# Kernel tuning notes

Measured on AMD Instinct MI355X. Metric: run time of the kernel, lower is better.

Reference implementation:

```python
import jax, jax.numpy as jnp
import numpy as np

B, T, ENC, DEC, OUT = 4096, 128, 128, 128, 1


def setup_inputs() -> dict:
    key = jax.random.key(0)
    ks = jax.random.split(key, 10)
    def s(k, shape, scale):
        return jax.random.normal(k, shape, jnp.float32) * scale
    return {
        "input_encoded": jax.random.normal(ks[0], (B, T, ENC), jnp.float32),
        "y_history": jax.random.normal(ks[1], (B, T - 1, OUT), jnp.float32),
        # attn_layer: Linear(2*DEC+ENC -> ENC), Tanh, Linear(ENC -> 1)
        "attn_W1": s(ks[2], (ENC, 2 * DEC + ENC), 0.05),
        "attn_b1": jnp.zeros((ENC,), jnp.float32),
        "attn_W2": s(ks[3], (1, ENC), 0.05),
        "attn_b2": jnp.zeros((1,), jnp.float32),
        # LSTM(input_size=OUT, hidden_size=DEC), gate order i,f,g,o
        "W_ih": s(ks[4], (4 * DEC, OUT), 0.08),
        "W_hh": s(ks[5], (4 * DEC, DEC), 0.08),
        "b_ih": jnp.zeros((4 * DEC,), jnp.float32),
        "b_hh": jnp.zeros((4 * DEC,), jnp.float32),
        # fc: Linear(ENC+OUT -> OUT), weight initialized with normal_() (std 1)
        "fc_W": s(ks[6], (OUT, ENC + OUT), 1.0),
        "fc_b": jnp.zeros((OUT,), jnp.float32),
        # fc_final: Linear(DEC+ENC -> OUT)
        "fc_final_W": s(ks[7], (OUT, DEC + ENC), 0.05),
        "fc_final_b": jnp.zeros((OUT,), jnp.float32),
    }


def reference(input_encoded, y_history, attn_W1, attn_b1, attn_W2, attn_b2,
              W_ih, W_hh, b_ih, b_hh, fc_W, fc_b, fc_final_W, fc_final_b):
    Bn, Tn, enc = input_encoded.shape
    dec = W_hh.shape[1]
    # Split attn first-layer weight into hidden / cell / encoded blocks so the
    # concat is never materialized; the encoder projection is loop-invariant.
    W1_h = attn_W1[:, :dec]
    W1_c = attn_W1[:, dec:2 * dec]
    W1_e = attn_W1[:, 2 * dec:]
    enc_proj = jnp.einsum('bte,he->bth', input_encoded, W1_e)  # [B,T,ENC]
    w2 = attn_W2[0]  # [ENC]

    def step(carry, y_t):
        h, c, _ = carry  # h,c: [B,DEC]
        hc_proj = h @ W1_h.T + c @ W1_c.T + attn_b1          # [B,ENC]
        e = jnp.tanh(enc_proj + hc_proj[:, None, :]) @ w2 + attn_b2[0]  # [B,T]
        beta = jax.nn.softmax(e, axis=1)
        context = jnp.einsum('bt,bte->be', beta, input_encoded)  # [B,ENC]
        y_tilde = jnp.concatenate([context, y_t], axis=1) @ fc_W.T + fc_b  # [B,OUT]
        gates = y_tilde @ W_ih.T + b_ih + h @ W_hh.T + b_hh    # [B,4*DEC]
        i, f, g, o = jnp.split(gates, 4, axis=1)
        c_new = jax.nn.sigmoid(f) * c + jax.nn.sigmoid(i) * jnp.tanh(g)
        h_new = jax.nn.sigmoid(o) * jnp.tanh(c_new)
        return (h_new, c_new, context), None

    h0 = jnp.zeros((Bn, dec), jnp.float32)
    c0 = jnp.zeros((Bn, dec), jnp.float32)
    ctx0 = jnp.zeros((Bn, enc), jnp.float32)
    (h, c, context), _ = jax.lax.scan(step, (h0, c0, ctx0),
                                      jnp.swapaxes(y_history, 0, 1))
    return jnp.concatenate([h, context], axis=1) @ fc_final_W.T + fc_final_b
```

## Files before the change

### kernel.cpp

```cpp
#include <hip/hip_runtime.h>
#include <stdint.h>

#define Bsz   4096
#define STEPS 127
#define NTH   512

typedef float    f4v __attribute__((ext_vector_type(4)));
typedef uint32_t u4v __attribute__((ext_vector_type(4)));
typedef _Float16 h2v __attribute__((ext_vector_type(2)));
typedef __fp16   g2v __attribute__((ext_vector_type(2)));

#define K2E  1.4426950408889634f
#define K2E2 2.8853900817779268f

__device__ __forceinline__ float rcp_f(float x) { return __builtin_amdgcn_rcpf(x); }
__device__ __forceinline__ float exp2_f(float x) {
#if __has_builtin(__builtin_amdgcn_exp2f)
    return __builtin_amdgcn_exp2f(x);
#else
    return exp2f(x);
#endif
}
__device__ __forceinline__ float sig_f(float x)  { return rcp_f(1.f + exp2_f(-K2E * x)); }
__device__ __forceinline__ float tanh_f(float x) { return 1.f - 2.f * rcp_f(1.f + exp2_f(K2E2 * x)); }
__device__ __forceinline__ uint32_t pkh2(float a, float b) {
    union { uint32_t u; g2v h; } v;
    v.h = __builtin_amdgcn_cvt_pkrtz(a, b);
    return v.u;
}
__device__ __forceinline__ float h2lo(uint32_t p) {
    union { uint32_t u; h2v h; } v; v.u = p; return (float)v.h[0];
}
__device__ __forceinline__ float h2hi(uint32_t p) {
    union { uint32_t u; h2v h; } v; v.u = p; return (float)v.h[1];
}
__device__ __forceinline__ float dot2(uint32_t a, uint32_t b, float c) {
    union { uint32_t u; h2v h; } x, y;
    x.u = a; y.u = b;
#if __has_builtin(__builtin_amdgcn_fdot2)
    return __builtin_amdgcn_fdot2(x.h, y.h, c, false);
#else
    return c + (float)x.h[0] * (float)y.h[0] + (float)x.h[1] * (float)y.h[1];
#endif
}

template<int CTRL, int RM, int BM>
__device__ __forceinline__ float dpp_add(float v) {
    union { float f; int i; } s, t;
    s.f = v;
    t.i = __builtin_amdgcn_update_dpp(0, s.i, CTRL, RM, BM, true);
    return v + t.f;
}
template<int CTRL>
__device__ __forceinline__ float dpp_mov(float v) {
    union { float f; int i; } s, t;
    s.f = v;
    t.i = __builtin_amdgcn_mov_dpp(s.i, CTRL, 0xf, 0xf, true);
    return t.f;
}
__device__ __forceinline__ float rd63(float v) {
    union { float f; int i; } s; s.f = v;
    union { int i; float f; } r; r.i = __builtin_amdgcn_readlane(s.i, 63);
    return r.f;
}
__device__ __forceinline__ float qsum(float v) {
    v = dpp_add<0xB1, 0xf, 0xf>(v);
    v = dpp_add<0x4E, 0xf, 0xf>(v);
    return v;
}
__device__ __forceinline__ float wsum(float v) {
    v = dpp_add<0x111, 0xf, 0xf>(v);
    v = dpp_add<0x112, 0xf, 0xf>(v);
    v = dpp_add<0x114, 0xf, 0xe>(v);
    v = dpp_add<0x118, 0xf, 0xc>(v);
    v = dpp_add<0x142, 0xa, 0xf>(v);
    v = dpp_add<0x143, 0xc, 0xf>(v);
    return rd63(v);
}

__global__ __launch_bounds__(NTH, 1)
void dec_kernel(const float* __restrict__ X,
                const float* __restrict__ yh,
                const float* __restrict__ W1,
                const float* __restrict__ b1,
                const float* __restrict__ W2,
                const float* __restrict__ b2u,
                const float* __restrict__ Wih,
                const float* __restrict__ Whh,
                const float* __restrict__ bih,
                const float* __restrict__ bhh,
                const float* __restrict__ fcW,
                const float* __restrict__ fcb,
                const float* __restrict__ Wff,
                const float* __restrict__ bff,
                float* __restrict__ out)
{
    const int tid  = threadIdx.x;
    const int lane = tid & 63;

    __shared__ __align__(16) uint32_t EPT_pk[128 * 68];
    __shared__ __align__(16) float    Xt[8][132];
    __shared__ __align__(16) uint32_t st2[2][144];
    __shared__ __align__(16) float    c32[2][128];
    __shared__ __align__(16) float    h32[128];
    __shared__ __align__(16) float    e_s[128];
    __shared__ __align__(16) float    hc2c[4][36];
    __shared__ __align__(16) float    w2m[4][36];
    __shared__ __align__(16) float    y_s[STEPS + 1];
    __shared__ __align__(16) float    XF[128];
    __shared__ __align__(16) float    XG[128];

    const float* Xb = X + (size_t)blockIdx.x * (128 * 128);

    if (tid < 288)   ((uint32_t*)st2)[tid] = 0u;
    if (tid < 128)   c32[0][tid] = 0.f;
    if (tid < STEPS) y_s[tid] = fcW[128] * yh[(size_t)blockIdx.x * STEPS + tid] + fcb[0];
    if (tid < 128)   w2m[tid >> 5][tid & 31] = -2.f * W2[tid];

    const int jA = tid >> 2;
    const int qA = tid & 3;

    {
        float aF = 0.f, aG = 0.f;
        #pragma unroll
        for (int u = 0; u < 8; ++u) {
            f4v xv = *(const f4v*)(Xb + jA * 128 + qA * 32 + 4 * u);
            f4v fv = *(const f4v*)(fcW + qA * 32 + 4 * u);
            f4v gv = *(const f4v*)(Wff + 128 + qA * 32 + 4 * u);
            aF += xv[0]*fv[0] + xv[1]*fv[1] + xv[2]*fv[2] + xv[3]*fv[3];
            aG += xv[0]*gv[0] + xv[1]*gv[1] + xv[2]*gv[2] + xv[3]*gv[3];
        }
        aF = qsum(aF);
        aG = qsum(aG);
        if (qA == 0) { XF[jA] = aF; XG[jA] = aG; }
    }

    {
        float w1e[32];
        #pragma unroll
        for (int u = 0; u < 8; ++u) {
            f4v w = *(const f4v*)(W1 + jA * 384 + 256 + qA * 32 + 4 * u);
            w1e[4*u] = w[0]; w1e[4*u+1] = w[1]; w1e[4*u+2] = w[2]; w1e[4*u+3] = w[3];
        }
        for (int tile = 0; tile < 16; ++tile) {
            __syncthreads();
            if (tid < 256) {
                int row = tid >> 5, c4 = tid & 31;
                int p = (c4 & 7) * 4 + (c4 >> 3);
                *(f4v*)&Xt[row][p * 4] = *(const f4v*)(Xb + (tile * 8 + row) * 128 + c4 * 4);
            }
            __syncthreads();
            #pragma unroll
            for (int tl = 0; tl < 8; ++tl) {
                float acc = 0.f;
                #pragma unroll
                for (int u = 0; u < 8; ++u) {
                    f4v xv = *(const f4v*)&Xt[tl][(u * 4 + qA) * 4];
                    acc += xv[0]*w1e[4*u] + xv[1]*w1e[4*u+1]
                         + xv[2]*w1e[4*u+2] + xv[3]*w1e[4*u+3];
                }
                acc = qsum(acc);
                float accp = __shfl_xor(acc, 4);
                if ((tid & 7) == 0)
                    EPT_pk[(tile * 8 + tl) * 68 + (tid >> 3)] = pkh2(acc, accp);
            }
        }
    }

    uint32_t w1pk[32];
    #pragma unroll
    for (int m = 0; m < 16; ++m) {
        f4v a = *(const f4v*)(W1 + jA * 384 + qA * 64 + 4 * m);
        w1pk[2*m]   = pkh2(a[0], a[1]);
        w1pk[2*m+1] = pkh2(a[2], a[3]);
    }
    const int jD = tid >> 2;
    const int r  = (tid & 3) * 128 + jD;
    uint32_t whh[64];
    #pragma unroll
    for (int m = 0; m < 32; ++m) {
        f4v w = *(const f4v*)(Whh + (size_t)r * 128 + 4 * m);
        whh[2*m]   = pkh2(w[0], w[1]);
        whh[2*m+1] = pkh2(w[2], w[3]);
    }
    const float wihv = Wih[r];
    const float bgv  = bih[r] + bhh[r];
    const float b1s  = K2E2 * b1[jA];
    float ytg_last = 0.f;
    __syncthreads();

    for (int s = 0; s < STEPS; ++s) {
        const int cur = s & 1;

        {
            float a0 = 0.f, a1 = 0.f;
            const uint32_t* sb = &st2[cur][qA * 36];
            #pragma unroll
            for (int u = 0; u < 8; ++u) {
                u4v sv = *(const u4v*)(sb + 4 * u);
                a0 = dot2(sv[0], w1pk[4*u],   a0);
                a1 = dot2(sv[1], w1pk[4*u+1], a1);
                a0 = dot2(sv[2], w1pk[4*u+2], a0);
                a1 = dot2(sv[3], w1pk[4*u+3], a1);
            }
            float acc = qsum(a0 + a1);
            if (qA == 0) hc2c[jA >> 5][jA & 31] = fmaf(K2E2, acc, b1s);
        }
        __syncthreads();

        {
            const int t = tid >> 2, q = tid & 3;
            const uint32_t* er = &EPT_pk[t * 68 + q * 16];
            u4v ee0 = *(const u4v*)(er);
            u4v ee1 = *(const u4v*)(er + 4);
            u4v ee2 = *(const u4v*)(er + 8);
            u4v ee3 = *(const u4v*)(er + 12);
            float acc = 0.f;
            #pragma unroll
            for (int u = 0; u < 4; ++u) {
                u4v ev = (u == 0) ? ee0 : (u == 1) ? ee1 : (u == 2) ? ee2 : ee3;
                f4v hcv = *(const f4v*)&hc2c[q][8 * u];
                f4v hcw = *(const f4v*)&hc2c[q][8 * u + 4];
                f4v wv  = *(const f4v*)&w2m[q][8 * u];
                f4v wvw = *(const f4v*)&w2m[q][8 * u + 4];
                #pragma unroll
                for (int m = 0; m < 4; ++m) {
                    uint32_t ep = ev[m];
                    float hl = (m < 2) ? hcv[2*m]   : hcw[2*m-4];
                    float hh = (m < 2) ? hcv[2*m+1] : hcw[2*m-3];
                    float wl = (m < 2) ? wv[2*m]    : wvw[2*m-4];
                    float wh = (m < 2) ? wv[2*m+1]  : wvw[2*m-3];
                    float z0 = exp2_f(fmaf(h2lo(ep), K2E2, hl));
                    float z1 = exp2_f(fmaf(h2hi(ep), K2E2, hh));
                    acc = fmaf(wl, rcp_f(1.f + z0), acc);
                    acc = fmaf(wh, rcp_f(1.f + z1), acc);
                }
            }
            acc = qsum(acc);
            if (q == 0) e_s[t] = acc;
        }
        __syncthreads();

        float ytc;
        {
            float v0 = e_s[lane], v1 = e_s[lane + 64];
            float p0 = exp2_f(K2E * v0), p1 = exp2_f(K2E * v1);
            float sp = wsum(p0 + p1);
            float sf = wsum(p0 * XF[lane] + p1 * XF[lane + 64]);
            float sg = wsum(p0 * XG[lane] + p1 * XG[lane + 64]);
            float inv = rcp_f(sp);
            ytc      = sf * inv;
            ytg_last = sg * inv;
        }

        {
            float yt = ytc + y_s[s];
            float d0 = 0.f, d1 = 0.f, d2 = 0.f, d3 = fmaf(wihv, yt, bgv);
            const uint32_t* hb = &st2[cur][0];
            #pragma unroll
            for (int m = 0; m < 8; ++m) {
                u4v sv = *(const u4v*)(hb + 4 * m);
                d0 = dot2(sv[0], whh[4*m],   d0);
                d1 = dot2(sv[1], whh[4*m+1], d1);
                d2 = dot2(sv[2], whh[4*m+2], d2);
                d3 = dot2(sv[3], whh[4*m+3], d3);
            }
            #pragma unroll
            for (int m = 0; m < 8; ++m) {
                u4v sv = *(const u4v*)(hb + 36 + 4 * m);
                d0 = dot2(sv[0], whh[32 + 4*m],   d0);
                d1 = dot2(sv[1], whh[32 + 4*m+1], d1);
                d2 = dot2(sv[2], whh[32 + 4*m+2], d2);
                d3 = dot2(sv[3], whh[32 + 4*m+3], d3);
            }
            float g  = (d0 + d1) + (d2 + d3);
            float gb = dpp_mov<0xB1>(g);
            float gc = dpp_mov<0x4E>(g);
            float gd = dpp_mov<0x4E>(gb);
            if ((tid & 3) == 0) {
                float co = c32[cur][jD];
                float cn = sig_f(gb) * co + sig_f(g) * tanh_f(gc);
                float hn = sig_f(gd) * tanh_f(cn);
                c32[cur ^ 1][jD] = cn;
                h32[jD] = hn;
                float hp = __shfl_xor(hn, 4);
                float cp = __shfl_xor(cn, 4);
                if ((tid & 7) == 0) {
                    int m0 = tid >> 3;
                    int sl = m0 + 4 * (m0 >> 5);
                    st2[cur ^ 1][sl]      = pkh2(hn, hp);
                    st2[cur ^ 1][72 + sl] = pkh2(cn, cp);
                }
            }
        }
        __syncthreads();
    }

    if (tid < 64) {
        float v = h32[lane] * Wff[lane] + h32[lane + 64] * Wff[lane + 64];
        v = wsum(v);
        if (lane == 0) out[blockIdx.x] = v + ytg_last + bff[0];
    }
}

extern "C" void kernel_launch(void* const* d_in, const int* in_sizes, int n_in,
                              void* d_out, int out_size, void* d_ws, size_t ws_size,
                              hipStream_t stream) {
    dec_kernel<<<Bsz, NTH, 0, stream>>>(
        (const float*)d_in[0],  (const float*)d_in[1],  (const float*)d_in[2],
        (const float*)d_in[3],  (const float*)d_in[4],  (const float*)d_in[5],
        (const float*)d_in[6],  (const float*)d_in[7],  (const float*)d_in[8],
        (const float*)d_in[9],  (const float*)d_in[10], (const float*)d_in[11],
        (const float*)d_in[12], (const float*)d_in[13], (float*)d_out);
}
```

Before: 5.190 ms.

## Process two batch rows per block and hoist W_hh dot before attention

Each workgroup now handles two batch elements, so per-block setup (weight register loads and fp16 packing) is amortised over two sequences and the per-step barriers are shared between them. The recurrent W_hh·h dot product moves into the first phase, next to the attention hidden projection, leaving only the input term to be added after the softmax. This halves the grid and roughly doubles LDS use per block (two EPT tables of about 35KB each), which may lower occupancy and lengthen each step's serial critical path.

Result: slower. 9.042 ms (+74.2%).

```diff
diff --git a/kernel.cpp b/kernel.cpp
--- a/kernel.cpp
+++ b/kernel.cpp
@@ -4,6 +4,7 @@
 #define Bsz   4096
 #define STEPS 127
 #define NTH   512
+#define NB    2
 
 typedef float    f4v __attribute__((ext_vector_type(4)));
 typedef uint32_t u4v __attribute__((ext_vector_type(4)));
@@ -98,29 +99,35 @@
     const int tid  = threadIdx.x;
     const int lane = tid & 63;
 
-    __shared__ __align__(16) uint32_t EPT_pk[128 * 68];
+    __shared__ __align__(16) uint32_t EPT_pk[NB][128 * 68];
     __shared__ __align__(16) float    Xt[8][132];
-    __shared__ __align__(16) uint32_t st2[2][144];
-    __shared__ __align__(16) float    c32[2][128];
-    __shared__ __align__(16) float    h32[128];
-    __shared__ __align__(16) float    e_s[128];
-    __shared__ __align__(16) float    hc2c[4][36];
+    __shared__ __align__(16) uint32_t st2[NB][2][144];
+    __shared__ __align__(16) float    c32[NB][2][128];
+    __shared__ __align__(16) float    h32[NB][128];
+    __shared__ __align__(16) float    e_s[NB][128];
+    __shared__ __align__(16) float    hc2c[NB][4][36];
     __shared__ __align__(16) float    w2m[4][36];
-    __shared__ __align__(16) float    y_s[STEPS + 1];
-    __shared__ __align__(16) float    XF[128];
-    __shared__ __align__(16) float    XG[128];
-
-    const float* Xb = X + (size_t)blockIdx.x * (128 * 128);
-
-    if (tid < 288)   ((uint32_t*)st2)[tid] = 0u;
-    if (tid < 128)   c32[0][tid] = 0.f;
-    if (tid < STEPS) y_s[tid] = fcW[128] * yh[(size_t)blockIdx.x * STEPS + tid] + fcb[0];
-    if (tid < 128)   w2m[tid >> 5][tid & 31] = -2.f * W2[tid];
+    __shared__ __align__(16) float    y_s[NB][STEPS + 1];
+    __shared__ __align__(16) float    XF[NB][128];
+    __shared__ __align__(16) float    XG[NB][128];
+
+    const float* Xb0 = X + (size_t)blockIdx.x * NB * (128 * 128);
+
+    #pragma unroll
+    for (int bb = 0; bb < NB; ++bb) {
+        if (tid < 288)   ((uint32_t*)st2[bb])[tid] = 0u;
+        if (tid < 128)   c32[bb][0][tid] = 0.f;
+        if (tid < STEPS) y_s[bb][tid] =
+            fcW[128] * yh[(size_t)(blockIdx.x * NB + bb) * STEPS + tid] + fcb[0];
+    }
+    if (tid < 128) w2m[tid >> 5][tid & 31] = -2.f * W2[tid];
 
     const int jA = tid >> 2;
     const int qA = tid & 3;
 
-    {
+    #pragma unroll
+    for (int bb = 0; bb < NB; ++bb) {
+        const float* Xb = Xb0 + bb * (128 * 128);
         float aF = 0.f, aG = 0.f;
         #pragma unroll
         for (int u = 0; u < 8; ++u) {
@@ -132,7 +139,7 @@
         }
         aF = qsum(aF);
         aG = qsum(aG);
-        if (qA == 0) { XF[jA] = aF; XG[jA] = aG; }
+        if (qA == 0) { XF[bb][jA] = aF; XG[bb][jA] = aG; }
     }
 
     {
@@ -142,27 +149,30 @@
             f4v w = *(const f4v*)(W1 + jA * 384 + 256 + qA * 32 + 4 * u);
             w1e[4*u] = w[0]; w1e[4*u+1] = w[1]; w1e[4*u+2] = w[2]; w1e[4*u+3] = w[3];
         }
-        for (int tile = 0; tile < 16; ++tile) {
-            __syncthreads();
-            if (tid < 256) {
-                int row = tid >> 5, c4 = tid & 31;
-                int p = (c4 & 7) * 4 + (c4 >> 3);
-                *(f4v*)&Xt[row][p * 4] = *(const f4v*)(Xb + (tile * 8 + row) * 128 + c4 * 4);
-            }
-            __syncthreads();
-            #pragma unroll
-            for (int tl = 0; tl < 8; ++tl) {
-                float acc = 0.f;
+        for (int bb = 0; bb < NB; ++bb) {
+            const float* Xb = Xb0 + bb * (128 * 128);
+            for (int tile = 0; tile < 16; ++tile) {
+                __syncthreads();
+                if (tid < 256) {
+                    int row = tid >> 5, c4 = tid & 31;
+                    int p = (c4 & 7) * 4 + (c4 >> 3);
+                    *(f4v*)&Xt[row][p * 4] = *(const f4v*)(Xb + (tile * 8 + row) * 128 + c4 * 4);
+                }
+                __syncthreads();
                 #pragma unroll
-                for (int u = 0; u < 8; ++u) {
-                    f4v xv = *(const f4v*)&Xt[tl][(u * 4 + qA) * 4];
-                    acc += xv[0]*w1e[4*u] + xv[1]*w1e[4*u+1]
-                         + xv[2]*w1e[4*u+2] + xv[3]*w1e[4*u+3];
+                for (int tl = 0; tl < 8; ++tl) {
+                    float acc = 0.f;
+                    #pragma unroll
+                    for (int u = 0; u < 8; ++u) {
+                        f4v xv = *(const f4v*)&Xt[tl][(u * 4 + qA) * 4];
+                        acc += xv[0]*w1e[4*u] + xv[1]*w1e[4*u+1]
+                             + xv[2]*w1e[4*u+2] + xv[3]*w1e[4*u+3];
+                    }
+                    acc = qsum(acc);
+                    float accp = __shfl_xor(acc, 4);
+                    if ((tid & 7) == 0)
+                        EPT_pk[bb][(tile * 8 + tl) * 68 + (tid >> 3)] = pkh2(acc, accp);
                 }
-                acc = qsum(acc);
-                float accp = __shfl_xor(acc, 4);
-                if ((tid & 7) == 0)
-                    EPT_pk[(tile * 8 + tl) * 68 + (tid >> 3)] = pkh2(acc, accp);
             }
         }
     }
@@ -186,15 +196,19 @@
     const float wihv = Wih[r];
     const float bgv  = bih[r] + bhh[r];
     const float b1s  = K2E2 * b1[jA];
-    float ytg_last = 0.f;
+    float ytg_last[NB];
+    #pragma unroll
+    for (int bb = 0; bb < NB; ++bb) ytg_last[bb] = 0.f;
     __syncthreads();
 
     for (int s = 0; s < STEPS; ++s) {
         const int cur = s & 1;
-
-        {
+        float gdot0, gdot1;
+
+        #pragma unroll
+        for (int bb = 0; bb < NB; ++bb) {
             float a0 = 0.f, a1 = 0.f;
-            const uint32_t* sb = &st2[cur][qA * 36];
+            const uint32_t* sb = &st2[bb][cur][qA * 36];
             #pragma unroll
             for (int u = 0; u < 8; ++u) {
                 u4v sv = *(const u4v*)(sb + 4 * u);
@@ -204,13 +218,35 @@
                 a1 = dot2(sv[3], w1pk[4*u+3], a1);
             }
             float acc = qsum(a0 + a1);
-            if (qA == 0) hc2c[jA >> 5][jA & 31] = fmaf(K2E2, acc, b1s);
+            if (qA == 0) hc2c[bb][jA >> 5][jA & 31] = fmaf(K2E2, acc, b1s);
+
+            float d0 = 0.f, d1 = 0.f, d2 = 0.f, d3 = 0.f;
+            const uint32_t* hb = &st2[bb][cur][0];
+            #pragma unroll
+            for (int m = 0; m < 8; ++m) {
+                u4v sv = *(const u4v*)(hb + 4 * m);
+                d0 = dot2(sv[0], whh[4*m],   d0);
+                d1 = dot2(sv[1], whh[4*m+1], d1);
+                d2 = dot2(sv[2], whh[4*m+2], d2);
+                d3 = dot2(sv[3], whh[4*m+3], d3);
+            }
+            #pragma unroll
+            for (int m = 0; m < 8; ++m) {
+                u4v sv = *(const u4v*)(hb + 36 + 4 * m);
+                d0 = dot2(sv[0], whh[32 + 4*m],   d0);
+                d1 = dot2(sv[1], whh[32 + 4*m+1], d1);
+                d2 = dot2(sv[2], whh[32 + 4*m+2], d2);
+                d3 = dot2(sv[3], whh[32 + 4*m+3], d3);
+            }
+            float gd = (d0 + d1) + (d2 + d3);
+            if (bb == 0) gdot0 = gd; else gdot1 = gd;
         }
         __syncthreads();
 
-        {
+        #pragma unroll
+        for (int bb = 0; bb < NB; ++bb) {
             const int t = tid >> 2, q = tid & 3;
-            const uint32_t* er = &EPT_pk[t * 68 + q * 16];
+            const uint32_t* er = &EPT_pk[bb][t * 68 + q * 16];
             u4v ee0 = *(const u4v*)(er);
             u4v ee1 = *(const u4v*)(er + 4);
             u4v ee2 = *(const u4v*)(er + 8);
@@ -219,8 +255,8 @@
             #pragma unroll
             for (int u = 0; u < 4; ++u) {
                 u4v ev = (u == 0) ? ee0 : (u == 1) ? ee1 : (u == 2) ? ee2 : ee3;
-                f4v hcv = *(const f4v*)&hc2c[q][8 * u];
-                f4v hcw = *(const f4v*)&hc2c[q][8 * u + 4];
+                f4v hcv = *(const f4v*)&hc2c[bb][q][8 * u];
+                f4v hcw = *(const f4v*)&hc2c[bb][q][8 * u + 4];
                 f4v wv  = *(const f4v*)&w2m[q][8 * u];
                 f4v wvw = *(const f4v*)&w2m[q][8 * u + 4];
                 #pragma unroll
@@ -237,59 +273,39 @@
                 }
             }
             acc = qsum(acc);
-            if (q == 0) e_s[t] = acc;
+            if (q == 0) e_s[bb][t] = acc;
         }
         __syncthreads();
 
-        float ytc;
-        {
-            float v0 = e_s[lane], v1 = e_s[lane + 64];
+        #pragma unroll
+        for (int bb = 0; bb < NB; ++bb) {
+            float v0 = e_s[bb][lane], v1 = e_s[bb][lane + 64];
             float p0 = exp2_f(K2E * v0), p1 = exp2_f(K2E * v1);
             float sp = wsum(p0 + p1);
-            float sf = wsum(p0 * XF[lane] + p1 * XF[lane + 64]);
-            float sg = wsum(p0 * XG[lane] + p1 * XG[lane + 64]);
+            float sf = wsum(p0 * XF[bb][lane] + p1 * XF[bb][lane + 64]);
+            float sg = wsum(p0 * XG[bb][lane] + p1 * XG[bb][lane + 64]);
             float inv = rcp_f(sp);
-            ytc      = sf * inv;
-            ytg_last = sg * inv;
-        }
-
-        {
-            float yt = ytc + y_s[s];
-            float d0 = 0.f, d1 = 0.f, d2 = 0.f, d3 = fmaf(wihv, yt, bgv);
-            const uint32_t* hb = &st2[cur][0];
-            #pragma unroll
-            for (int m = 0; m < 8; ++m) {
-                u4v sv = *(const u4v*)(hb + 4 * m);
-                d0 = dot2(sv[0], whh[4*m],   d0);
-                d1 = dot2(sv[1], whh[4*m+1], d1);
-                d2 = dot2(sv[2], whh[4*m+2], d2);
-                d3 = dot2(sv[3], whh[4*m+3], d3);
-            }
-            #pragma unroll
-            for (int m = 0; m < 8; ++m) {
-                u4v sv = *(const u4v*)(hb + 36 + 4 * m);
-                d0 = dot2(sv[0], whh[32 + 4*m],   d0);
-                d1 = dot2(sv[1], whh[32 + 4*m+1], d1);
-                d2 = dot2(sv[2], whh[32 + 4*m+2], d2);
-                d3 = dot2(sv[3], whh[32 + 4*m+3], d3);
-            }
-            float g  = (d0 + d1) + (d2 + d3);
+            float ytc = sf * inv;
+            ytg_last[bb] = sg * inv;
+
+            float yt = ytc + y_s[bb][s];
+            float g  = ((bb == 0) ? gdot0 : gdot1) + fmaf(wihv, yt, bgv);
             float gb = dpp_mov<0xB1>(g);
             float gc = dpp_mov<0x4E>(g);
             float gd = dpp_mov<0x4E>(gb);
             if ((tid & 3) == 0) {
-                float co = c32[cur][jD];
+                float co = c32[bb][cur][jD];
                 float cn = sig_f(gb) * co + sig_f(g) * tanh_f(gc);
                 float hn = sig_f(gd) * tanh_f(cn);
-                c32[cur ^ 1][jD] = cn;
-                h32[jD] = hn;
+                c32[bb][cur ^ 1][jD] = cn;
+                h32[bb][jD] = hn;
                 float hp = __shfl_xor(hn, 4);
                 float cp = __shfl_xor(cn, 4);
                 if ((tid & 7) == 0) {
                     int m0 = tid >> 3;
                     int sl = m0 + 4 * (m0 >> 5);
-                    st2[cur ^ 1][sl]      = pkh2(hn, hp);
-                    st2[cur ^ 1][72 + sl] = pkh2(cn, cp);
+                    st2[bb][cur ^ 1][sl]      = pkh2(hn, hp);
+                    st2[bb][cur ^ 1][72 + sl] = pkh2(cn, cp);
                 }
             }
         }
@@ -297,16 +313,19 @@
     }
 
     if (tid < 64) {
-        float v = h32[lane] * Wff[lane] + h32[lane + 64] * Wff[lane + 64];
-        v = wsum(v);
-        if (lane == 0) out[blockIdx.x] = v + ytg_last + bff[0];
+        #pragma unroll
+        for (int bb = 0; bb < NB; ++bb) {
+            float v = h32[bb][lane] * Wff[lane] + h32[bb][lane + 64] * Wff[lane + 64];
+            v = wsum(v);
+            if (lane == 0) out[blockIdx.x * NB + bb] = v + ytg_last[bb] + bff[0];
+        }
     }
 }
 
 extern "C" void kernel_launch(void* const* d_in, const int* in_sizes, int n_in,
                               void* d_out, int out_size, void* d_ws, size_t ws_size,
                               hipStream_t stream) {
-    dec_kernel<<<Bsz, NTH, 0, stream>>>(
+    dec_kernel<<<Bsz / NB, NTH, 0, stream>>>(
         (const float*)d_in[0],  (const float*)d_in[1],  (const float*)d_in[2],
         (const float*)d_in[3],  (const float*)d_in[4],  (const float*)d_in[5],
         (const float*)d_in[6],  (const float*)d_in[7],  (const float*)d_in[8],
```

## Pack two batch elements per 1024-thread workgroup

Applied to the files above, without the earlier changes.

Each workgroup now processes two independent batch rows, with 512 threads per row, and all shared buffers are duplicated per half. The launch uses half as many blocks, with flat work group size 1024 and waves_per_eu(4). The aim is to raise resident waves per CU so one sequence's step latency and barriers can overlap with the other's work. In exchange, the shared barriers now couple the two rows, and the register budget per thread is tighter, which may cause spills given the large per-thread weight arrays (whh 64, w1pk 32).

New measurement: 11.96 ms. 2.3x slower.

```diff
diff --git a/kernel.cpp b/kernel.cpp
--- a/kernel.cpp
+++ b/kernel.cpp
@@ -3,7 +3,8 @@
 
 #define Bsz   4096
 #define STEPS 127
-#define NTH   512
+#define NTH   1024
+#define NB    2
 
 typedef float    f4v __attribute__((ext_vector_type(4)));
 typedef uint32_t u4v __attribute__((ext_vector_type(4)));
@@ -78,7 +79,8 @@
     return rd63(v);
 }
 
-__global__ __launch_bounds__(NTH, 1)
+__global__ __attribute__((amdgpu_flat_work_group_size(NTH, NTH)))
+           __attribute__((amdgpu_waves_per_eu(4)))
 void dec_kernel(const float* __restrict__ X,
                 const float* __restrict__ yh,
                 const float* __restrict__ W1,
@@ -96,29 +98,32 @@
                 float* __restrict__ out)
 {
     const int tid  = threadIdx.x;
+    const int half = tid >> 9;
+    const int t    = tid & 511;
     const int lane = tid & 63;
 
-    __shared__ __align__(16) uint32_t EPT_pk[128 * 68];
-    __shared__ __align__(16) float    Xt[8][132];
-    __shared__ __align__(16) uint32_t st2[2][144];
-    __shared__ __align__(16) float    c32[2][128];
-    __shared__ __align__(16) float    h32[128];
-    __shared__ __align__(16) float    e_s[128];
-    __shared__ __align__(16) float    hc2c[4][36];
+    __shared__ __align__(16) uint32_t EPT_pk[NB][128 * 68];
+    __shared__ __align__(16) float    Xt[NB][8][132];
+    __shared__ __align__(16) uint32_t st2[NB][2][144];
+    __shared__ __align__(16) float    c32[NB][2][128];
+    __shared__ __align__(16) float    h32[NB][128];
+    __shared__ __align__(16) float    e_s[NB][128];
+    __shared__ __align__(16) float    hc2c[NB][4][36];
     __shared__ __align__(16) float    w2m[4][36];
-    __shared__ __align__(16) float    y_s[STEPS + 1];
-    __shared__ __align__(16) float    XF[128];
-    __shared__ __align__(16) float    XG[128];
-
-    const float* Xb = X + (size_t)blockIdx.x * (128 * 128);
-
-    if (tid < 288)   ((uint32_t*)st2)[tid] = 0u;
-    if (tid < 128)   c32[0][tid] = 0.f;
-    if (tid < STEPS) y_s[tid] = fcW[128] * yh[(size_t)blockIdx.x * STEPS + tid] + fcb[0];
-    if (tid < 128)   w2m[tid >> 5][tid & 31] = -2.f * W2[tid];
-
-    const int jA = tid >> 2;
-    const int qA = tid & 3;
+    __shared__ __align__(16) float    y_s[NB][STEPS + 1];
+    __shared__ __align__(16) float    XF[NB][128];
+    __shared__ __align__(16) float    XG[NB][128];
+
+    const float* Xb = X + (size_t)(blockIdx.x * NB + half) * (128 * 128);
+
+    if (t < 288)   ((uint32_t*)st2[half])[t] = 0u;
+    if (t < 128)   c32[half][0][t] = 0.f;
+    if (t < STEPS) y_s[half][t] =
+        fcW[128] * yh[(size_t)(blockIdx.x * NB + half) * STEPS + t] + fcb[0];
+    if (tid < 128) w2m[tid >> 5][tid & 31] = -2.f * W2[tid];
+
+    const int jA = t >> 2;
+    const int qA = t & 3;
 
     {
         float aF = 0.f, aG = 0.f;
@@ -132,7 +137,7 @@
         }
         aF = qsum(aF);
         aG = qsum(aG);
-        if (qA == 0) { XF[jA] = aF; XG[jA] = aG; }
+        if (qA == 0) { XF[half][jA] = aF; XG[half][jA] = aG; }
     }
 
     {
@@ -144,10 +149,10 @@
         }
         for (int tile = 0; tile < 16; ++tile) {
             __syncthreads();
-            if (tid < 256) {
-                int row = tid >> 5, c4 = tid & 31;
+            if (t < 256) {
+                int row = t >> 5, c4 = t & 31;
                 int p = (c4 & 7) * 4 + (c4 >> 3);
-                *(f4v*)&Xt[row][p * 4] = *(const f4v*)(Xb + (tile * 8 + row) * 128 + c4 * 4);
+                *(f4v*)&Xt[half][row][p * 4] = *(const f4v*)(Xb + (tile * 8 + row) * 128 + c4 * 4);
             }
             __syncthreads();
             #pragma unroll
@@ -155,14 +160,14 @@
                 float acc = 0.f;
                 #pragma unroll
                 for (int u = 0; u < 8; ++u) {
-                    f4v xv = *(const f4v*)&Xt[tl][(u * 4 + qA) * 4];
+                    f4v xv = *(const f4v*)&Xt[half][tl][(u * 4 + qA) * 4];
                     acc += xv[0]*w1e[4*u] + xv[1]*w1e[4*u+1]
                          + xv[2]*w1e[4*u+2] + xv[3]*w1e[4*u+3];
                 }
                 acc = qsum(acc);
                 float accp = __shfl_xor(acc, 4);
-                if ((tid & 7) == 0)
-                    EPT_pk[(tile * 8 + tl) * 68 + (tid >> 3)] = pkh2(acc, accp);
+                if ((t & 7) == 0)
+                    EPT_pk[half][(tile * 8 + tl) * 68 + (t >> 3)] = pkh2(acc, accp);
             }
         }
     }
@@ -174,8 +179,8 @@
         w1pk[2*m]   = pkh2(a[0], a[1]);
         w1pk[2*m+1] = pkh2(a[2], a[3]);
     }
-    const int jD = tid >> 2;
-    const int r  = (tid & 3) * 128 + jD;
+    const int jD = t >> 2;
+    const int r  = (t & 3) * 128 + jD;
     uint32_t whh[64];
     #pragma unroll
     for (int m = 0; m < 32; ++m) {
@@ -194,7 +199,7 @@
 
         {
             float a0 = 0.f, a1 = 0.f;
-            const uint32_t* sb = &st2[cur][qA * 36];
+            const uint32_t* sb = &st2[half][cur][qA * 36];
             #pragma unroll
             for (int u = 0; u < 8; ++u) {
                 u4v sv = *(const u4v*)(sb + 4 * u);
@@ -204,13 +209,13 @@
                 a1 = dot2(sv[3], w1pk[4*u+3], a1);
             }
             float acc = qsum(a0 + a1);
-            if (qA == 0) hc2c[jA >> 5][jA & 31] = fmaf(K2E2, acc, b1s);
+            if (qA == 0) hc2c[half][jA >> 5][jA & 31] = fmaf(K2E2, acc, b1s);
         }
         __syncthreads();
 
         {
-            const int t = tid >> 2, q = tid & 3;
-            const uint32_t* er = &EPT_pk[t * 68 + q * 16];
+            const int tt = t >> 2, q = t & 3;
+            const uint32_t* er = &EPT_pk[half][tt * 68 + q * 16];
             u4v ee0 = *(const u4v*)(er);
             u4v ee1 = *(const u4v*)(er + 4);
             u4v ee2 = *(const u4v*)(er + 8);
@@ -219,8 +224,8 @@
             #pragma unroll
             for (int u = 0; u < 4; ++u) {
                 u4v ev = (u == 0) ? ee0 : (u == 1) ? ee1 : (u == 2) ? ee2 : ee3;
-                f4v hcv = *(const f4v*)&hc2c[q][8 * u];
-                f4v hcw = *(const f4v*)&hc2c[q][8 * u + 4];
+                f4v hcv = *(const f4v*)&hc2c[half][q][8 * u];
+                f4v hcw = *(const f4v*)&hc2c[half][q][8 * u + 4];
                 f4v wv  = *(const f4v*)&w2m[q][8 * u];
                 f4v wvw = *(const f4v*)&w2m[q][8 * u + 4];
                 #pragma unroll
@@ -237,26 +242,26 @@
                 }
             }
             acc = qsum(acc);
-            if (q == 0) e_s[t] = acc;
+            if (q == 0) e_s[half][tt] = acc;
         }
         __syncthreads();
 
         float ytc;
         {
-            float v0 = e_s[lane], v1 = e_s[lane + 64];
+            float v0 = e_s[half][lane], v1 = e_s[half][lane + 64];
             float p0 = exp2_f(K2E * v0), p1 = exp2_f(K2E * v1);
             float sp = wsum(p0 + p1);
-            float sf = wsum(p0 * XF[lane] + p1 * XF[lane + 64]);
-            float sg = wsum(p0 * XG[lane] + p1 * XG[lane + 64]);
+            float sf = wsum(p0 * XF[half][lane] + p1 * XF[half][lane + 64]);
+            float sg = wsum(p0 * XG[half][lane] + p1 * XG[half][lane + 64]);
             float inv = rcp_f(sp);
             ytc      = sf * inv;
             ytg_last = sg * inv;
         }
 
         {
-            float yt = ytc + y_s[s];
+            float yt = ytc + y_s[half][s];
             float d0 = 0.f, d1 = 0.f, d2 = 0.f, d3 = fmaf(wihv, yt, bgv);
-            const uint32_t* hb = &st2[cur][0];
+            const uint32_t* hb = &st2[half][cur][0];
             #pragma unroll
             for (int m = 0; m < 8; ++m) {
                 u4v sv = *(const u4v*)(hb + 4 * m);
@@ -277,36 +282,36 @@
             float gb = dpp_mov<0xB1>(g);
             float gc = dpp_mov<0x4E>(g);
             float gd = dpp_mov<0x4E>(gb);
-            if ((tid & 3) == 0) {
-                float co = c32[cur][jD];
+            if ((t & 3) == 0) {
+                float co = c32[half][cur][jD];
                 float cn = sig_f(gb) * co + sig_f(g) * tanh_f(gc);
                 float hn = sig_f(gd) * tanh_f(cn);
-                c32[cur ^ 1][jD] = cn;
-                h32[jD] = hn;
+                c32[half][cur ^ 1][jD] = cn;
+                h32[half][jD] = hn;
                 float hp = __shfl_xor(hn, 4);
                 float cp = __shfl_xor(cn, 4);
-                if ((tid & 7) == 0) {
-                    int m0 = tid >> 3;
+                if ((t & 7) == 0) {
+                    int m0 = t >> 3;
                     int sl = m0 + 4 * (m0 >> 5);
-                    st2[cur ^ 1][sl]      = pkh2(hn, hp);
-                    st2[cur ^ 1][72 + sl] = pkh2(cn, cp);
+                    st2[half][cur ^ 1][sl]      = pkh2(hn, hp);
+                    st2[half][cur ^ 1][72 + sl] = pkh2(cn, cp);
                 }
             }
         }
         __syncthreads();
     }
 
-    if (tid < 64) {
-        float v = h32[lane] * Wff[lane] + h32[lane + 64] * Wff[lane + 64];
+    if (t < 64) {
+        float v = h32[half][lane] * Wff[lane] + h32[half][lane + 64] * Wff[lane + 64];
         v = wsum(v);
-        if (lane == 0) out[blockIdx.x] = v + ytg_last + bff[0];
+        if (lane == 0) out[blockIdx.x * NB + half] = v + ytg_last + bff[0];
     }
 }
 
 extern "C" void kernel_launch(void* const* d_in, const int* in_sizes, int n_in,
                               void* d_out, int out_size, void* d_ws, size_t ws_size,
                               hipStream_t stream) {
-    dec_kernel<<<Bsz, NTH, 0, stream>>>(
+    dec_kernel<<<Bsz / NB, NTH, 0, stream>>>(
         (const float*)d_in[0],  (const float*)d_in[1],  (const float*)d_in[2],
         (const float*)d_in[3],  (const float*)d_in[4],  (const float*)d_in[5],
         (const float*)d_in[6],  (const float*)d_in[7],  (const float*)d_in[8],
```

## Compute attention tanh in fp16 and hoist W_hh dot ahead of softmax

Applied to the files above, without the earlier changes.

Moves the attention energy inner loop (exp2 and reciprocal of the tanh form) to packed fp16 arithmetic, with the hidden/cell projection and W2 weights stored as packed halves and the encoder projection prescaled by the exp2 constant. It also moves the recurrent W_hh dot product into the first phase, before the softmax barrier, so the gate accumulation overlaps with earlier work and the LSTM update only adds the input term. The softmax exponent moves into the energy phase. This reduces the fp32 transcendental load and shortens the serial chain, but fp16 accumulation over 32 terms risks precision loss.

Measured after the change: 5.331 ms. +2.7%, slower.

```diff
diff --git a/kernel.cpp b/kernel.cpp
--- a/kernel.cpp
+++ b/kernel.cpp
@@ -12,6 +12,8 @@
 
 #define K2E  1.4426950408889634f
 #define K2E2 2.8853900817779268f
+
+extern "C" __device__ _Float16 __ocml_exp2_f16(_Float16);
 
 __device__ __forceinline__ float rcp_f(float x) { return __builtin_amdgcn_rcpf(x); }
 __device__ __forceinline__ float exp2_f(float x) {
@@ -21,6 +23,14 @@
     return exp2f(x);
 #endif
 }
+__device__ __forceinline__ _Float16 rcp_h(_Float16 x) {
+#if __has_builtin(__builtin_amdgcn_rcph)
+    return __builtin_amdgcn_rcph(x);
+#else
+    return (_Float16)rcp_f((float)x);
+#endif
+}
+__device__ __forceinline__ _Float16 exp2_h(_Float16 x) { return __ocml_exp2_f16(x); }
 __device__ __forceinline__ float sig_f(float x)  { return rcp_f(1.f + exp2_f(-K2E * x)); }
 __device__ __forceinline__ float tanh_f(float x) { return 1.f - 2.f * rcp_f(1.f + exp2_f(K2E2 * x)); }
 __device__ __forceinline__ uint32_t pkh2(float a, float b) {
@@ -28,11 +38,8 @@
     v.h = __builtin_amdgcn_cvt_pkrtz(a, b);
     return v.u;
 }
-__device__ __forceinline__ float h2lo(uint32_t p) {
-    union { uint32_t u; h2v h; } v; v.u = p; return (float)v.h[0];
-}
-__device__ __forceinline__ float h2hi(uint32_t p) {
-    union { uint32_t u; h2v h; } v; v.u = p; return (float)v.h[1];
+__device__ __forceinline__ h2v uh(uint32_t u) {
+    union { uint32_t u; h2v h; } v; v.u = u; return v.h;
 }
 __device__ __forceinline__ float dot2(uint32_t a, uint32_t b, float c) {
     union { uint32_t u; h2v h; } x, y;
@@ -103,9 +110,9 @@
     __shared__ __align__(16) uint32_t st2[2][144];
     __shared__ __align__(16) float    c32[2][128];
     __shared__ __align__(16) float    h32[128];
-    __shared__ __align__(16) float    e_s[128];
-    __shared__ __align__(16) float    hc2c[4][36];
-    __shared__ __align__(16) float    w2m[4][36];
+    __shared__ __align__(16) float    p_s[128];
+    __shared__ __align__(16) uint32_t hc2pk[68];
+    __shared__ __align__(16) uint32_t w2pk[68];
     __shared__ __align__(16) float    y_s[STEPS + 1];
     __shared__ __align__(16) float    XF[128];
     __shared__ __align__(16) float    XG[128];
@@ -115,7 +122,7 @@
     if (tid < 288)   ((uint32_t*)st2)[tid] = 0u;
     if (tid < 128)   c32[0][tid] = 0.f;
     if (tid < STEPS) y_s[tid] = fcW[128] * yh[(size_t)blockIdx.x * STEPS + tid] + fcb[0];
-    if (tid < 128)   w2m[tid >> 5][tid & 31] = -2.f * W2[tid];
+    if (tid < 64)    w2pk[tid] = pkh2(-2.f * W2[2 * tid], -2.f * W2[2 * tid + 1]);
 
     const int jA = tid >> 2;
     const int qA = tid & 3;
@@ -159,7 +166,7 @@
                     acc += xv[0]*w1e[4*u] + xv[1]*w1e[4*u+1]
                          + xv[2]*w1e[4*u+2] + xv[3]*w1e[4*u+3];
                 }
-                acc = qsum(acc);
+                acc = K2E2 * qsum(acc);
                 float accp = __shfl_xor(acc, 4);
                 if ((tid & 7) == 0)
                     EPT_pk[(tile * 8 + tl) * 68 + (tid >> 3)] = pkh2(acc, accp);
@@ -186,11 +193,14 @@
     const float wihv = Wih[r];
     const float bgv  = bih[r] + bhh[r];
     const float b1s  = K2E2 * b1[jA];
+    const int   tB   = tid >> 2;
+    const int   qB   = tid & 3;
     float ytg_last = 0.f;
     __syncthreads();
 
     for (int s = 0; s < STEPS; ++s) {
         const int cur = s & 1;
+        float gdot;
 
         {
             float a0 = 0.f, a1 = 0.f;
@@ -203,59 +213,11 @@
                 a0 = dot2(sv[2], w1pk[4*u+2], a0);
                 a1 = dot2(sv[3], w1pk[4*u+3], a1);
             }
-            float acc = qsum(a0 + a1);
-            if (qA == 0) hc2c[jA >> 5][jA & 31] = fmaf(K2E2, acc, b1s);
-        }
-        __syncthreads();
-
-        {
-            const int t = tid >> 2, q = tid & 3;
-            const uint32_t* er = &EPT_pk[t * 68 + q * 16];
-            u4v ee0 = *(const u4v*)(er);
-            u4v ee1 = *(const u4v*)(er + 4);
-            u4v ee2 = *(const u4v*)(er + 8);
-            u4v ee3 = *(const u4v*)(er + 12);
-            float acc = 0.f;
-            #pragma unroll
-            for (int u = 0; u < 4; ++u) {
-                u4v ev = (u == 0) ? ee0 : (u == 1) ? ee1 : (u == 2) ? ee2 : ee3;
-                f4v hcv = *(const f4v*)&hc2c[q][8 * u];
-                f4v hcw = *(const f4v*)&hc2c[q][8 * u + 4];
-                f4v wv  = *(const f4v*)&w2m[q][8 * u];
-                f4v wvw = *(const f4v*)&w2m[q][8 * u + 4];
-                #pragma unroll
-                for (int m = 0; m < 4; ++m) {
-                    uint32_t ep = ev[m];
-                    float hl = (m < 2) ? hcv[2*m]   : hcw[2*m-4];
-                    float hh = (m < 2) ? hcv[2*m+1] : hcw[2*m-3];
-                    float wl = (m < 2) ? wv[2*m]    : wvw[2*m-4];
-                    float wh = (m < 2) ? wv[2*m+1]  : wvw[2*m-3];
-                    float z0 = exp2_f(fmaf(h2lo(ep), K2E2, hl));
-                    float z1 = exp2_f(fmaf(h2hi(ep), K2E2, hh));
-                    acc = fmaf(wl, rcp_f(1.f + z0), acc);
-                    acc = fmaf(wh, rcp_f(1.f + z1), acc);
-                }
-            }
-            acc = qsum(acc);
-            if (q == 0) e_s[t] = acc;
-        }
-        __syncthreads();
-
-        float ytc;
-        {
-            float v0 = e_s[lane], v1 = e_s[lane + 64];
-            float p0 = exp2_f(K2E * v0), p1 = exp2_f(K2E * v1);
-            float sp = wsum(p0 + p1);
-            float sf = wsum(p0 * XF[lane] + p1 * XF[lane + 64]);
-            float sg = wsum(p0 * XG[lane] + p1 * XG[lane + 64]);
-            float inv = rcp_f(sp);
-            ytc      = sf * inv;
-            ytg_last = sg * inv;
-        }
-
-        {
-            float yt = ytc + y_s[s];
-            float d0 = 0.f, d1 = 0.f, d2 = 0.f, d3 = fmaf(wihv, yt, bgv);
+            float val = fmaf(K2E2, qsum(a0 + a1), b1s);
+            float valp = __shfl_xor(val, 4);
+            if ((tid & 7) == 0) hc2pk[tid >> 3] = pkh2(val, valp);
+
+            float d0 = 0.f, d1 = 0.f, d2 = 0.f, d3 = 0.f;
             const uint32_t* hb = &st2[cur][0];
             #pragma unroll
             for (int m = 0; m < 8; ++m) {
@@ -273,7 +235,48 @@
                 d2 = dot2(sv[2], whh[32 + 4*m+2], d2);
                 d3 = dot2(sv[3], whh[32 + 4*m+3], d3);
             }
-            float g  = (d0 + d1) + (d2 + d3);
+            gdot = (d0 + d1) + (d2 + d3);
+        }
+        __syncthreads();
+
+        {
+            const uint32_t* er = &EPT_pk[tB * 68 + qB * 16];
+            const uint32_t* hr = &hc2pk[qB * 16];
+            const uint32_t* wr = &w2pk[qB * 16];
+            _Float16 accL = (_Float16)0.f, accH = (_Float16)0.f;
+            const _Float16 one = (_Float16)1.f;
+            #pragma unroll
+            for (int u = 0; u < 4; ++u) {
+                u4v ev = *(const u4v*)(er + 4 * u);
+                u4v hv = *(const u4v*)(hr + 4 * u);
+                u4v wv = *(const u4v*)(wr + 4 * u);
+                #pragma unroll
+                for (int m = 0; m < 4; ++m) {
+                    h2v z  = uh(ev[m]) + uh(hv[m]);
+                    h2v w2 = uh(wv[m]);
+                    _Float16 p0 = exp2_h(z[0]);
+                    _Float16 p1 = exp2_h(z[1]);
+                    accL += w2[0] * rcp_h(one + p0);
+                    accH += w2[1] * rcp_h(one + p1);
+                }
+            }
+            float e = qsum((float)accL + (float)accH);
+            float pt = exp2_f(K2E * e);
+            if (qB == 0) p_s[tB] = pt;
+        }
+        __syncthreads();
+
+        {
+            float v0 = p_s[lane], v1 = p_s[lane + 64];
+            float sp = wsum(v0 + v1);
+            float sf = wsum(v0 * XF[lane] + v1 * XF[lane + 64]);
+            float sg = wsum(v0 * XG[lane] + v1 * XG[lane + 64]);
+            float inv = rcp_f(sp);
+            float ytc = sf * inv;
+            ytg_last  = sg * inv;
+
+            float yt = ytc + y_s[s];
+            float g  = gdot + fmaf(wihv, yt, bgv);
             float gb = dpp_mov<0xB1>(g);
             float gc = dpp_mov<0x4E>(g);
             float gd = dpp_mov<0x4E>(gb);
```
